# Optimization experiments

Measured on AMD Instinct MI355X. Metric: run time of the kernel, lower is better.

## Reference

```python
import jax, jax.numpy as jnp
import numpy as np

N, F, HID, C = 8192, 256, 128, 64
ALPHA = 0.2  # LeakyReLU negative slope
NEG = -9e15  # mask value from the torch code


def xavier(key, shape, gain=1.414):
    fan_in, fan_out = shape[0], shape[1]
    limit = gain * np.sqrt(6.0 / (fan_in + fan_out))
    return jax.random.uniform(key, shape, jnp.float32, -limit, limit)


def setup_inputs() -> dict:
    key = jax.random.key(0)
    ks = jax.random.split(key, 6)
    features = jax.random.normal(ks[0], (N, F), jnp.float32)
    support = (jax.random.uniform(ks[1], (N, N)) > 0.995).astype(jnp.float32)
    support = support.at[jnp.arange(N), jnp.arange(N)].set(1.0)
    W0 = xavier(ks[2], (2 * F, HID))
    a0 = xavier(ks[3], (2 * HID, 1))
    W1 = xavier(ks[4], (2 * HID, C))
    a1 = xavier(ks[5], (2 * C, 1))
    return {"features": features, "support": support, "W0": W0, "a0": a0, "W1": W1, "a1": a1}


def gat_layer(x, adj, W, a, concat):
    # precalc=False branch: support = spmm(adj, x); cat with x
    s = adj @ x                               # (N, Fin)
    sup = jnp.concatenate([s, x], axis=1)     # (N, 2*Fin)
    h = sup @ W                               # (N, Fout)
    Fout = h.shape[1]
    # cat([h_i, h_j]) @ a == h_i @ a[:Fout] + h_j @ a[Fout:]  (same math, no N*N*2F tensor)
    src = h @ a[:Fout, 0]                     # (N,)
    dst = h @ a[Fout:, 0]                     # (N,)
    e = jax.nn.leaky_relu(src[:, None] + dst[None, :], ALPHA)  # (N, N)
    e = jnp.where(adj > 0, e, NEG)            # adjacency-masked scores
    att = jax.nn.softmax(e, axis=1)           # (N, N); dropout is identity in eval
    hp = att @ h                              # (N, Fout)
    return jax.nn.elu(hp) if concat else hp


def reference(features, support, W0, a0, W1, a1):
    x = gat_layer(features, support, W0, a0, concat=True)
    out = gat_layer(x, support, W1, a1, concat=False)
    return jax.nn.log_softmax(out, axis=1)
```

## Files before the change

kernel.cpp:

```cpp
#include <hip/hip_runtime.h>
#include <math.h>

#define NROWS 8192
#define EDGE_CAP 128

__global__ __launch_bounds__(256) void fused_csr_gemm1(const float* __restrict__ adj,
                                                       int* __restrict__ cnt,
                                                       int* __restrict__ col,
                                                       const float* __restrict__ A,
                                                       const float* __restrict__ W,
                                                       float* __restrict__ Y,
                                                       float* __restrict__ Z) {
    __shared__ float As[16][64];
    __shared__ float Bs[16][128];
    int gb  = blockIdx.x;
    int tid = threadIdx.x;

    if (gb < 256) {
        int bm = gb & 127, bn = gb >> 7;
        int tx = tid & 15, ty = tid >> 4;
        const float* Wb = W + (size_t)bn * 256 * 128;
        float acc[4][8] = {};
        for (int k0 = 0; k0 < 256; k0 += 16) {
            {
                int r = tid >> 2, kk = (tid & 3) * 4;
                float4 v = *(const float4*)&A[(size_t)(bm * 64 + r) * 256 + k0 + kk];
                As[kk + 0][r] = v.x; As[kk + 1][r] = v.y;
                As[kk + 2][r] = v.z; As[kk + 3][r] = v.w;
            }
            {
                int kk = tid >> 4, c = (tid & 15) * 8;
                *(float4*)&Bs[kk][c]     = *(const float4*)&Wb[(size_t)(k0 + kk) * 128 + c];
                *(float4*)&Bs[kk][c + 4] = *(const float4*)&Wb[(size_t)(k0 + kk) * 128 + c + 4];
            }
            __syncthreads();
            #pragma unroll
            for (int kk = 0; kk < 16; ++kk) {
                float a[4], b[8];
                #pragma unroll
                for (int i = 0; i < 4; ++i) a[i] = As[kk][ty * 4 + i];
                #pragma unroll
                for (int j = 0; j < 8; ++j) b[j] = Bs[kk][tx * 8 + j];
                #pragma unroll
                for (int i = 0; i < 4; ++i)
                    #pragma unroll
                    for (int j = 0; j < 8; ++j) acc[i][j] += a[i] * b[j];
            }
            __syncthreads();
        }
        float* O = bn ? Z : Y;
        #pragma unroll
        for (int i = 0; i < 4; ++i) {
            int r = bm * 64 + ty * 4 + i;
            float4 v0 = {acc[i][0], acc[i][1], acc[i][2], acc[i][3]};
            float4 v1 = {acc[i][4], acc[i][5], acc[i][6], acc[i][7]};
            *(float4*)&O[(size_t)r * 128 + tx * 8]     = v0;
            *(float4*)&O[(size_t)r * 128 + tx * 8 + 4] = v1;
        }
    } else {
        int row  = (gb - 256) * 4 + (tid >> 6);
        int lane = tid & 63;
        const float4* arow = (const float4*)(adj + (size_t)row * NROWS);
        int* crow = col + (size_t)row * EDGE_CAP;
        int count = 0;
        for (int it = 0; it < NROWS / 256; ++it) {
            float4 v = arow[it * 64 + lane];
            float vv[4] = {v.x, v.y, v.z, v.w};
            #pragma unroll
            for (int p = 0; p < 4; ++p) {
                bool nz = vv[p] > 0.0f;
                unsigned long long m = __ballot(nz);
                if (nz) {
                    int off = count + __popcll(m & ((1ull << lane) - 1ull));
                    if (off < EDGE_CAP) crow[off] = it * 256 + lane * 4 + p;
                }
                count += __popcll(m);
            }
        }
        if (lane == 0) cnt[row] = count < EDGE_CAP ? count : EDGE_CAP;
    }
}

template <int KD, int FOUT>
__global__ __launch_bounds__(256) void gemm_split(const float* __restrict__ A,
                                                  const float* __restrict__ W,
                                                  float* __restrict__ Y,
                                                  float* __restrict__ Z) {
    const int BK = 16;
    __shared__ float As[BK][64];
    __shared__ float Bs[BK][64];
    int bm = blockIdx.x, bn = blockIdx.y;
    int tid = threadIdx.x;
    int tx = tid & 15, ty = tid >> 4;
    const bool half = (bn * 64) >= FOUT;
    const float* Wb = half ? W + (size_t)KD * FOUT - FOUT : W;
    float acc[4][4] = {};
    for (int k0 = 0; k0 < KD; k0 += BK) {
        {
            int r  = tid >> 2;
            int kk = (tid & 3) * 4;
            float4 v = *(const float4*)&A[(size_t)(bm * 64 + r) * KD + k0 + kk];
            As[kk + 0][r] = v.x; As[kk + 1][r] = v.y;
            As[kk + 2][r] = v.z; As[kk + 3][r] = v.w;
        }
        {
            int kk = tid >> 4;
            int n4 = (tid & 15) * 4;
            *(float4*)&Bs[kk][n4] =
                *(const float4*)&Wb[(size_t)(k0 + kk) * FOUT + bn * 64 + n4];
        }
        __syncthreads();
        #pragma unroll
        for (int kk = 0; kk < BK; ++kk) {
            float a[4], b[4];
            #pragma unroll
            for (int i = 0; i < 4; ++i) a[i] = As[kk][ty * 4 + i];
            #pragma unroll
            for (int i = 0; i < 4; ++i) b[i] = Bs[kk][tx * 4 + i];
            #pragma unroll
            for (int i = 0; i < 4; ++i)
                #pragma unroll
                for (int j = 0; j < 4; ++j) acc[i][j] += a[i] * b[j];
        }
        __syncthreads();
    }
    float* O = half ? Z : Y;
    int col0 = bn * 64 + tx * 4 - (half ? FOUT : 0);
    #pragma unroll
    for (int i = 0; i < 4; ++i) {
        int r = bm * 64 + ty * 4 + i;
        float4 v = {acc[i][0], acc[i][1], acc[i][2], acc[i][3]};
        *(float4*)&O[(size_t)r * FOUT + col0] = v;
    }
}

template <int FOUT>
__global__ __launch_bounds__(256) void spmm_add_scores(const int* __restrict__ cnt,
                                                       const int* __restrict__ col,
                                                       const float* __restrict__ Y,
                                                       const float* __restrict__ Z,
                                                       const float* __restrict__ a,
                                                       float* __restrict__ H,
                                                       float* __restrict__ src,
                                                       float* __restrict__ dst) {
    __shared__ int sbuf[4][EDGE_CAP];
    int wav  = threadIdx.x >> 6;
    int lane = threadIdx.x & 63;
    int row  = blockIdx.x * 4 + wav;
    int n    = cnt[row];
    const int* cr = col + (size_t)row * EDGE_CAP;
    for (int e = lane; e < n; e += 64) sbuf[wav][e] = cr[e];

    float s1, s2;
    if constexpr (FOUT == 128) {
        const float2* Y2 = (const float2*)Y;
        float2 s = {0.0f, 0.0f};
        int e = 0;
        for (; e + 8 <= n; e += 8) {
            float2 v[8];
            #pragma unroll
            for (int u = 0; u < 8; ++u) {
                int j = sbuf[wav][e + u];
                v[u] = Y2[(size_t)j * 64 + lane];
            }
            #pragma unroll
            for (int u = 0; u < 8; ++u) { s.x += v[u].x; s.y += v[u].y; }
        }
        for (; e < n; ++e) {
            int j = sbuf[wav][e];
            float2 v = Y2[(size_t)j * 64 + lane];
            s.x += v.x; s.y += v.y;
        }
        float2 z = ((const float2*)Z)[(size_t)row * 64 + lane];
        float hx = s.x + z.x, hy = s.y + z.y;
        float2 hv = {hx, hy};
        ((float2*)H)[(size_t)row * 64 + lane] = hv;
        s1 = hx * a[lane * 2] + hy * a[lane * 2 + 1];
        s2 = hx * a[FOUT + lane * 2] + hy * a[FOUT + lane * 2 + 1];
    } else {
        float s = 0.0f;
        int e = 0;
        for (; e + 8 <= n; e += 8) {
            float v[8];
            #pragma unroll
            for (int u = 0; u < 8; ++u) v[u] = Y[(size_t)sbuf[wav][e + u] * 64 + lane];
            #pragma unroll
            for (int u = 0; u < 8; ++u) s += v[u];
        }
        for (; e < n; ++e) s += Y[(size_t)sbuf[wav][e] * 64 + lane];
        float h = s + Z[(size_t)row * 64 + lane];
        H[(size_t)row * 64 + lane] = h;
        s1 = h * a[lane];
        s2 = h * a[FOUT + lane];
    }
    #pragma unroll
    for (int off = 32; off; off >>= 1) {
        s1 += __shfl_xor(s1, off);
        s2 += __shfl_xor(s2, off);
    }
    if (lane == 0) { src[row] = s1; dst[row] = s2; }
}

template <int FOUT, int MODE>
__global__ __launch_bounds__(256) void attn_aggregate(const int* __restrict__ cnt,
                                                      const int* __restrict__ col,
                                                      const float* __restrict__ H,
                                                      const float* __restrict__ src,
                                                      const float* __restrict__ dst,
                                                      float* __restrict__ out) {
    __shared__ float pbuf[4][EDGE_CAP];
    __shared__ int   cbuf[4][EDGE_CAP];
    int wav  = threadIdx.x >> 6;
    int lane = threadIdx.x & 63;
    int row  = blockIdx.x * 4 + wav;
    int n    = cnt[row];
    const int* cr = col + (size_t)row * EDGE_CAP;
    float si = src[row];

    float m = -3.0e38f;
    for (int e = lane; e < n; e += 64) {
        int j = cr[e];
        float x = si + dst[j];
        x = x > 0.0f ? x : 0.2f * x;
        cbuf[wav][e] = j;
        pbuf[wav][e] = x;
        m = fmaxf(m, x);
    }
    #pragma unroll
    for (int off = 32; off; off >>= 1) m = fmaxf(m, __shfl_xor(m, off));

    float ssum = 0.0f;
    for (int e = lane; e < n; e += 64) {
        float p = __expf(pbuf[wav][e] - m);
        pbuf[wav][e] = p;
        ssum += p;
    }
    #pragma unroll
    for (int off = 32; off; off >>= 1) ssum += __shfl_xor(ssum, off);
    float inv = 1.0f / ssum;

    if constexpr (FOUT == 128) {
        const float2* H2 = (const float2*)H;
        float2 o = {0.0f, 0.0f};
        int e = 0;
        for (; e + 8 <= n; e += 8) {
            float2 v[8]; float p[8];
            #pragma unroll
            for (int u = 0; u < 8; ++u) {
                int j = cbuf[wav][e + u];
                p[u] = pbuf[wav][e + u];
                v[u] = H2[(size_t)j * 64 + lane];
            }
            #pragma unroll
            for (int u = 0; u < 8; ++u) { o.x += p[u] * v[u].x; o.y += p[u] * v[u].y; }
        }
        for (; e < n; ++e) {
            int j = cbuf[wav][e];
            float p = pbuf[wav][e];
            float2 v = H2[(size_t)j * 64 + lane];
            o.x += p * v.x; o.y += p * v.y;
        }
        float vx = o.x * inv, vy = o.y * inv;
        vx = vx > 0.0f ? vx : (__expf(vx) - 1.0f);
        vy = vy > 0.0f ? vy : (__expf(vy) - 1.0f);
        float2 ov = {vx, vy};
        ((float2*)out)[(size_t)row * 64 + lane] = ov;
    } else {
        float o = 0.0f;
        int e = 0;
        for (; e + 8 <= n; e += 8) {
            float v[8]; float p[8];
            #pragma unroll
            for (int u = 0; u < 8; ++u) {
                p[u] = pbuf[wav][e + u];
                v[u] = H[(size_t)cbuf[wav][e + u] * 64 + lane];
            }
            #pragma unroll
            for (int u = 0; u < 8; ++u) o += p[u] * v[u];
        }
        for (; e < n; ++e) o += pbuf[wav][e] * H[(size_t)cbuf[wav][e] * 64 + lane];
        float logit = o * inv;
        float mm = logit;
        #pragma unroll
        for (int off = 32; off; off >>= 1) mm = fmaxf(mm, __shfl_xor(mm, off));
        float se = __expf(logit - mm);
        #pragma unroll
        for (int off = 32; off; off >>= 1) se += __shfl_xor(se, off);
        out[(size_t)row * 64 + lane] = logit - mm - logf(se);
    }
}

extern "C" void kernel_launch(void* const* d_in, const int* in_sizes, int n_in,
                              void* d_out, int out_size, void* d_ws, size_t ws_size,
                              hipStream_t stream) {
    const float* feat = (const float*)d_in[0];
    const float* adj  = (const float*)d_in[1];
    const float* W0   = (const float*)d_in[2];
    const float* a0   = (const float*)d_in[3];
    const float* W1   = (const float*)d_in[4];
    const float* a1   = (const float*)d_in[5];
    float* out = (float*)d_out;

    char* w = (char*)d_ws;
    int* cnt = (int*)w;                w += (size_t)NROWS * sizeof(int);
    int* col = (int*)w;                w += (size_t)NROWS * EDGE_CAP * sizeof(int);
    float* Y1   = (float*)w;           w += (size_t)NROWS * 128 * sizeof(float);
    float* Z1   = (float*)w;           w += (size_t)NROWS * 128 * sizeof(float);
    float* H1   = (float*)w;           w += (size_t)NROWS * 128 * sizeof(float);
    float* src1 = (float*)w;           w += (size_t)NROWS * sizeof(float);
    float* dst1 = (float*)w;           w += (size_t)NROWS * sizeof(float);
    float* X1   = (float*)w;           w += (size_t)NROWS * 128 * sizeof(float);
    float* Y2   = (float*)w;           w += (size_t)NROWS * 64 * sizeof(float);
    float* Z2   = (float*)w;           w += (size_t)NROWS * 64 * sizeof(float);
    float* H2   = (float*)w;           w += (size_t)NROWS * 64 * sizeof(float);
    float* src2 = (float*)w;           w += (size_t)NROWS * sizeof(float);
    float* dst2 = (float*)w;           w += (size_t)NROWS * sizeof(float);

    fused_csr_gemm1<<<256 + NROWS / 4, 256, 0, stream>>>(adj, cnt, col, feat, W0, Y1, Z1);

    spmm_add_scores<128><<<NROWS / 4, 256, 0, stream>>>(cnt, col, Y1, Z1, a0, H1, src1, dst1);
    attn_aggregate<128, 0><<<NROWS / 4, 256, 0, stream>>>(cnt, col, H1, src1, dst1, X1);

    {
        dim3 g(NROWS / 64, 2 * 64 / 64);
        gemm_split<128, 64><<<g, 256, 0, stream>>>(X1, W1, Y2, Z2);
    }
    spmm_add_scores<64><<<NROWS / 4, 256, 0, stream>>>(cnt, col, Y2, Z2, a1, H2, src2, dst2);
    attn_aggregate<64, 1><<<NROWS / 4, 256, 0, stream>>>(cnt, col, H2, src2, dst2, out);
}
```

Measured before the change: 438.2 us.

## Fuse layer-1 attention aggregation with layer-2 GEMM and use nontemporal adjacency loads

Folds the second-layer projection (X1 @ W1 split into Y2/Z2) into the layer-1 attention aggregation kernel. Each wave stages its ELU output row in shared memory and does a 128x64 matvec against W1. This removes the X1 intermediate buffer and one kernel launch. It also switches the dense adjacency scan to nontemporal loads so the 256MB stream does not pollute cache. The trade-off is that the per-row matvec rereads W1 from cache for every row instead of using a tiled GEMM with reuse.

```diff
diff --git a/kernel.cpp b/kernel.cpp
--- a/kernel.cpp
+++ b/kernel.cpp
@@ -3,6 +3,8 @@
 
 #define NROWS 8192
 #define EDGE_CAP 128
+
+using f4v = __attribute__((ext_vector_type(4))) float;
 
 __global__ __launch_bounds__(256) void fused_csr_gemm1(const float* __restrict__ adj,
                                                        int* __restrict__ cnt,
@@ -60,11 +62,11 @@
     } else {
         int row  = (gb - 256) * 4 + (tid >> 6);
         int lane = tid & 63;
-        const float4* arow = (const float4*)(adj + (size_t)row * NROWS);
+        const f4v* arow = (const f4v*)(adj + (size_t)row * NROWS);
         int* crow = col + (size_t)row * EDGE_CAP;
         int count = 0;
         for (int it = 0; it < NROWS / 256; ++it) {
-            float4 v = arow[it * 64 + lane];
+            f4v v = __builtin_nontemporal_load(&arow[it * 64 + lane]);
             float vv[4] = {v.x, v.y, v.z, v.w};
             #pragma unroll
             for (int p = 0; p < 4; ++p) {
@@ -78,59 +80,6 @@
             }
         }
         if (lane == 0) cnt[row] = count < EDGE_CAP ? count : EDGE_CAP;
-    }
-}
-
-template <int KD, int FOUT>
-__global__ __launch_bounds__(256) void gemm_split(const float* __restrict__ A,
-                                                  const float* __restrict__ W,
-                                                  float* __restrict__ Y,
-                                                  float* __restrict__ Z) {
-    const int BK = 16;
-    __shared__ float As[BK][64];
-    __shared__ float Bs[BK][64];
-    int bm = blockIdx.x, bn = blockIdx.y;
-    int tid = threadIdx.x;
-    int tx = tid & 15, ty = tid >> 4;
-    const bool half = (bn * 64) >= FOUT;
-    const float* Wb = half ? W + (size_t)KD * FOUT - FOUT : W;
-    float acc[4][4] = {};
-    for (int k0 = 0; k0 < KD; k0 += BK) {
-        {
-            int r  = tid >> 2;
-            int kk = (tid & 3) * 4;
-            float4 v = *(const float4*)&A[(size_t)(bm * 64 + r) * KD + k0 + kk];
-            As[kk + 0][r] = v.x; As[kk + 1][r] = v.y;
-            As[kk + 2][r] = v.z; As[kk + 3][r] = v.w;
-        }
-        {
-            int kk = tid >> 4;
-            int n4 = (tid & 15) * 4;
-            *(float4*)&Bs[kk][n4] =
-                *(const float4*)&Wb[(size_t)(k0 + kk) * FOUT + bn * 64 + n4];
-        }
-        __syncthreads();
-        #pragma unroll
-        for (int kk = 0; kk < BK; ++kk) {
-            float a[4], b[4];
-            #pragma unroll
-            for (int i = 0; i < 4; ++i) a[i] = As[kk][ty * 4 + i];
-            #pragma unroll
-            for (int i = 0; i < 4; ++i) b[i] = Bs[kk][tx * 4 + i];
-            #pragma unroll
-            for (int i = 0; i < 4; ++i)
-                #pragma unroll
-                for (int j = 0; j < 4; ++j) acc[i][j] += a[i] * b[j];
-        }
-        __syncthreads();
-    }
-    float* O = half ? Z : Y;
-    int col0 = bn * 64 + tx * 4 - (half ? FOUT : 0);
-    #pragma unroll
-    for (int i = 0; i < 4; ++i) {
-        int r = bm * 64 + ty * 4 + i;
-        float4 v = {acc[i][0], acc[i][1], acc[i][2], acc[i][3]};
-        *(float4*)&O[(size_t)r * FOUT + col0] = v;
     }
 }
 
@@ -201,8 +150,85 @@
     if (lane == 0) { src[row] = s1; dst[row] = s2; }
 }
 
-template <int FOUT, int MODE>
-__global__ __launch_bounds__(256) void attn_aggregate(const int* __restrict__ cnt,
+__global__ __launch_bounds__(256) void attn_agg_gemm2(const int* __restrict__ cnt,
+                                                      const int* __restrict__ col,
+                                                      const float* __restrict__ H,
+                                                      const float* __restrict__ src,
+                                                      const float* __restrict__ dst,
+                                                      const float* __restrict__ W1,
+                                                      float* __restrict__ Y2,
+                                                      float* __restrict__ Z2) {
+    __shared__ float pbuf[4][EDGE_CAP];
+    __shared__ int   cbuf[4][EDGE_CAP];
+    __shared__ float xrow[4][128];
+    int wav  = threadIdx.x >> 6;
+    int lane = threadIdx.x & 63;
+    int row  = blockIdx.x * 4 + wav;
+    int n    = cnt[row];
+    const int* cr = col + (size_t)row * EDGE_CAP;
+    float si = src[row];
+
+    float m = -3.0e38f;
+    for (int e = lane; e < n; e += 64) {
+        int j = cr[e];
+        float x = si + dst[j];
+        x = x > 0.0f ? x : 0.2f * x;
+        cbuf[wav][e] = j;
+        pbuf[wav][e] = x;
+        m = fmaxf(m, x);
+    }
+    #pragma unroll
+    for (int off = 32; off; off >>= 1) m = fmaxf(m, __shfl_xor(m, off));
+
+    float ssum = 0.0f;
+    for (int e = lane; e < n; e += 64) {
+        float p = __expf(pbuf[wav][e] - m);
+        pbuf[wav][e] = p;
+        ssum += p;
+    }
+    #pragma unroll
+    for (int off = 32; off; off >>= 1) ssum += __shfl_xor(ssum, off);
+    float inv = 1.0f / ssum;
+
+    const float2* H2 = (const float2*)H;
+    float2 o = {0.0f, 0.0f};
+    int e = 0;
+    for (; e + 8 <= n; e += 8) {
+        float2 v[8]; float p[8];
+        #pragma unroll
+        for (int u = 0; u < 8; ++u) {
+            int j = cbuf[wav][e + u];
+            p[u] = pbuf[wav][e + u];
+            v[u] = H2[(size_t)j * 64 + lane];
+        }
+        #pragma unroll
+        for (int u = 0; u < 8; ++u) { o.x += p[u] * v[u].x; o.y += p[u] * v[u].y; }
+    }
+    for (; e < n; ++e) {
+        int j = cbuf[wav][e];
+        float p = pbuf[wav][e];
+        float2 v = H2[(size_t)j * 64 + lane];
+        o.x += p * v.x; o.y += p * v.y;
+    }
+    float vx = o.x * inv, vy = o.y * inv;
+    vx = vx > 0.0f ? vx : (__expf(vx) - 1.0f);
+    vy = vy > 0.0f ? vy : (__expf(vy) - 1.0f);
+
+    float2 hv = {vx, vy};
+    ((float2*)&xrow[wav][0])[lane] = hv;
+
+    float y = 0.0f, z = 0.0f;
+    #pragma unroll 8
+    for (int k = 0; k < 128; ++k) {
+        float xk = xrow[wav][k];
+        y += xk * W1[(size_t)k * 64 + lane];
+        z += xk * W1[(size_t)(128 + k) * 64 + lane];
+    }
+    Y2[(size_t)row * 64 + lane] = y;
+    Z2[(size_t)row * 64 + lane] = z;
+}
+
+__global__ __launch_bounds__(256) void attn_agg_final(const int* __restrict__ cnt,
                                                       const int* __restrict__ col,
                                                       const float* __restrict__ H,
                                                       const float* __restrict__ src,
@@ -239,55 +265,28 @@
     for (int off = 32; off; off >>= 1) ssum += __shfl_xor(ssum, off);
     float inv = 1.0f / ssum;
 
-    if constexpr (FOUT == 128) {
-        const float2* H2 = (const float2*)H;
-        float2 o = {0.0f, 0.0f};
-        int e = 0;
-        for (; e + 8 <= n; e += 8) {
-            float2 v[8]; float p[8];
-            #pragma unroll
-            for (int u = 0; u < 8; ++u) {
-                int j = cbuf[wav][e + u];
-                p[u] = pbuf[wav][e + u];
-                v[u] = H2[(size_t)j * 64 + lane];
-            }
-            #pragma unroll
-            for (int u = 0; u < 8; ++u) { o.x += p[u] * v[u].x; o.y += p[u] * v[u].y; }
-        }
-        for (; e < n; ++e) {
-            int j = cbuf[wav][e];
-            float p = pbuf[wav][e];
-            float2 v = H2[(size_t)j * 64 + lane];
-            o.x += p * v.x; o.y += p * v.y;
-        }
-        float vx = o.x * inv, vy = o.y * inv;
-        vx = vx > 0.0f ? vx : (__expf(vx) - 1.0f);
-        vy = vy > 0.0f ? vy : (__expf(vy) - 1.0f);
-        float2 ov = {vx, vy};
-        ((float2*)out)[(size_t)row * 64 + lane] = ov;
-    } else {
-        float o = 0.0f;
-        int e = 0;
-        for (; e + 8 <= n; e += 8) {
-            float v[8]; float p[8];
-            #pragma unroll
-            for (int u = 0; u < 8; ++u) {
-                p[u] = pbuf[wav][e + u];
-                v[u] = H[(size_t)cbuf[wav][e + u] * 64 + lane];
-            }
-            #pragma unroll
-            for (int u = 0; u < 8; ++u) o += p[u] * v[u];
-        }
-        for (; e < n; ++e) o += pbuf[wav][e] * H[(size_t)cbuf[wav][e] * 64 + lane];
-        float logit = o * inv;
-        float mm = logit;
-        #pragma unroll
-        for (int off = 32; off; off >>= 1) mm = fmaxf(mm, __shfl_xor(mm, off));
-        float se = __expf(logit - mm);
-        #pragma unroll
-        for (int off = 32; off; off >>= 1) se += __shfl_xor(se, off);
-        out[(size_t)row * 64 + lane] = logit - mm - logf(se);
-    }
+    float o = 0.0f;
+    int e = 0;
+    for (; e + 8 <= n; e += 8) {
+        float v[8]; float p[8];
+        #pragma unroll
+        for (int u = 0; u < 8; ++u) {
+            p[u] = pbuf[wav][e + u];
+            v[u] = H[(size_t)cbuf[wav][e + u] * 64 + lane];
+        }
+        #pragma unroll
+        for (int u = 0; u < 8; ++u) o += p[u] * v[u];
+    }
+    for (; e < n; ++e) o += pbuf[wav][e] * H[(size_t)cbuf[wav][e] * 64 + lane];
+
+    float logit = o * inv;
+    float mm = logit;
+    #pragma unroll
+    for (int off = 32; off; off >>= 1) mm = fmaxf(mm, __shfl_xor(mm, off));
+    float se = __expf(logit - mm);
+    #pragma unroll
+    for (int off = 32; off; off >>= 1) se += __shfl_xor(se, off);
+    out[(size_t)row * 64 + lane] = logit - mm - logf(se);
 }
 
 extern "C" void kernel_launch(void* const* d_in, const int* in_sizes, int n_in,
@@ -309,7 +308,6 @@
     float* H1   = (float*)w;           w += (size_t)NROWS * 128 * sizeof(float);
     float* src1 = (float*)w;           w += (size_t)NROWS * sizeof(float);
     float* dst1 = (float*)w;           w += (size_t)NROWS * sizeof(float);
-    float* X1   = (float*)w;           w += (size_t)NROWS * 128 * sizeof(float);
     float* Y2   = (float*)w;           w += (size_t)NROWS * 64 * sizeof(float);
     float* Z2   = (float*)w;           w += (size_t)NROWS * 64 * sizeof(float);
     float* H2   = (float*)w;           w += (size_t)NROWS * 64 * sizeof(float);
@@ -319,12 +317,8 @@
     fused_csr_gemm1<<<256 + NROWS / 4, 256, 0, stream>>>(adj, cnt, col, feat, W0, Y1, Z1);
 
     spmm_add_scores<128><<<NROWS / 4, 256, 0, stream>>>(cnt, col, Y1, Z1, a0, H1, src1, dst1);
-    attn_aggregate<128, 0><<<NROWS / 4, 256, 0, stream>>>(cnt, col, H1, src1, dst1, X1);
-
-    {
-        dim3 g(NROWS / 64, 2 * 64 / 64);
-        gemm_split<128, 64><<<g, 256, 0, stream>>>(X1, W1, Y2, Z2);
-    }
+    attn_agg_gemm2<<<NROWS / 4, 256, 0, stream>>>(cnt, col, H1, src1, dst1, W1, Y2, Z2);
+
     spmm_add_scores<64><<<NROWS / 4, 256, 0, stream>>>(cnt, col, Y2, Z2, a1, H2, src2, dst2);
-    attn_aggregate<64, 1><<<NROWS / 4, 256, 0, stream>>>(cnt, col, H2, src2, dst2, out);
-}
+    attn_agg_final<<<NROWS / 4, 256, 0, stream>>>(cnt, col, H2, src2, dst2, out);
+}
```

Result: no change. 432.5 us (-1.3%).
